# Kernel tuning notes

Hardware: AMD Instinct MI355X
Metric: run time of the kernel (lower is better)

Reference implementation:

```python
import jax, jax.numpy as jnp
import numpy as np

D_MODEL = 1024
N_HEADS = 16
HEAD_DIM = D_MODEL // N_HEADS
FF_DIM = 4096
EPS = 1e-5


def _layer_norm(v, g, b):
    mu = jnp.mean(v, axis=-1, keepdims=True)
    var = jnp.mean(jnp.square(v - mu), axis=-1, keepdims=True)
    return (v - mu) * jax.lax.rsqrt(var + EPS) * g + b


def setup_inputs() -> dict:
    key = jax.random.key(0)
    ks = jax.random.split(key, 16)
    s = 0.02
    x = jax.random.normal(ks[0], (2, 2048, D_MODEL), dtype=jnp.float32)
    Wq = jax.random.normal(ks[1], (D_MODEL, D_MODEL), dtype=jnp.float32) * s
    Wk = jax.random.normal(ks[2], (D_MODEL, D_MODEL), dtype=jnp.float32) * s
    Wv = jax.random.normal(ks[3], (D_MODEL, D_MODEL), dtype=jnp.float32) * s
    Wo = jax.random.normal(ks[4], (D_MODEL, D_MODEL), dtype=jnp.float32) * s
    bq = jnp.zeros((D_MODEL,), jnp.float32)
    bk = jnp.zeros((D_MODEL,), jnp.float32)
    bv = jnp.zeros((D_MODEL,), jnp.float32)
    bo = jnp.zeros((D_MODEL,), jnp.float32)
    # per-head Conv1d(kernel=1) == per-head linear; weights [H, out, in]
    W1 = jax.random.normal(ks[5], (N_HEADS, FF_DIM, HEAD_DIM), dtype=jnp.float32) * s
    b1 = jnp.zeros((N_HEADS, FF_DIM), jnp.float32)
    W2 = jax.random.normal(ks[6], (N_HEADS, HEAD_DIM, FF_DIM), dtype=jnp.float32) * s
    b2 = jnp.zeros((N_HEADS, HEAD_DIM), jnp.float32)
    g1 = jnp.ones((D_MODEL,), jnp.float32)
    be1 = jnp.zeros((D_MODEL,), jnp.float32)
    g2 = jnp.ones((D_MODEL,), jnp.float32)
    be2 = jnp.zeros((D_MODEL,), jnp.float32)
    return {"x": x, "Wq": Wq, "bq": bq, "Wk": Wk, "bk": bk, "Wv": Wv, "bv": bv,
            "Wo": Wo, "bo": bo, "W1": W1, "b1": b1, "W2": W2, "b2": b2,
            "g1": g1, "be1": be1, "g2": g2, "be2": be2}


def reference(x, Wq, bq, Wk, bk, Wv, bv, Wo, bo, W1, b1, W2, b2, g1, be1, g2, be2):
    B, S, D = x.shape
    H, hd = N_HEADS, HEAD_DIM
    # --- multi-head self-attention (standard scaled dot-product) ---
    q = (x @ Wq + bq).reshape(B, S, H, hd)
    k = (x @ Wk + bk).reshape(B, S, H, hd)
    v = (x @ Wv + bv).reshape(B, S, H, hd)
    scores = jnp.einsum('bqhd,bkhd->bhqk', q, k) / jnp.sqrt(jnp.float32(hd))
    attn = jax.nn.softmax(scores, axis=-1)          # [B,H,S,S]
    ctx = jnp.einsum('bhqk,bkhd->bqhd', attn, v).reshape(B, S, D)
    residual = ctx @ Wo + bo
    # dropout is identity in eval mode
    x1 = _layer_norm(x + residual, g1, be1)
    # --- per-head feed-forward (Conv1d kernel=1 per head, batched over heads) ---
    xh = x1.reshape(B, S, H, hd)
    h = jax.nn.relu(jnp.einsum('bshd,hfd->bshf', xh, W1) + b1)   # [B,S,H,FF]
    ff = jnp.einsum('bshf,hdf->bshd', h, W2) + b2                 # [B,S,H,hd]
    y = _layer_norm(x1 + ff.reshape(B, S, D), g2, be2)
    return (y, attn)
```

## Files before the change

### kernel.cpp

```cpp
#include <hip/hip_runtime.h>
#include <cstddef>

#define D_M 1024
#define NH 16
#define HD 64
#define FFD 4096
#define SQ 2048
#define BB 2
#define TOK (BB*SQ)
#define EPS 1e-5f

typedef __attribute__((ext_vector_type(8))) short bf16x8;
typedef __attribute__((ext_vector_type(4))) float f32x4;

__device__ inline unsigned short f32_bf16_rne(float f) {
  unsigned int u = __float_as_uint(f);
  unsigned int r = (u + 0x7fffu + ((u >> 16) & 1u)) >> 16;
  return (unsigned short)r;
}

__device__ inline float wave_sum(float v) {
  #pragma unroll
  for (int m = 32; m >= 1; m >>= 1) v += __shfl_xor(v, m);
  return v;
}

__global__ __launch_bounds__(256)
void convert2_bf16_k(const float* __restrict__ s0, unsigned short* __restrict__ d0,
                     const float* __restrict__ s1, unsigned short* __restrict__ d1, int n4) {
  const float* src = blockIdx.y ? s1 : s0;
  unsigned short* dst = blockIdx.y ? d1 : d0;
  int i = blockIdx.x * 256 + threadIdx.x;
  if (i >= n4) return;
  float4 v = ((const float4*)src)[i];
  ushort4 h;
  h.x = f32_bf16_rne(v.x); h.y = f32_bf16_rne(v.y);
  h.z = f32_bf16_rne(v.z); h.w = f32_bf16_rne(v.w);
  ((ushort4*)dst)[i] = h;
}

__global__ __launch_bounds__(256)
void convert_bf16_k(const float* __restrict__ src, unsigned short* __restrict__ dst, int n4) {
  int i = blockIdx.x * 256 + threadIdx.x;
  if (i >= n4) return;
  float4 v = ((const float4*)src)[i];
  ushort4 h;
  h.x = f32_bf16_rne(v.x); h.y = f32_bf16_rne(v.y);
  h.z = f32_bf16_rne(v.z); h.w = f32_bf16_rne(v.w);
  ((ushort4*)dst)[i] = h;
}

__global__ __launch_bounds__(256)
void transp4_k(const float* __restrict__ W0, const float* __restrict__ W1_,
               const float* __restrict__ W2_, const float* __restrict__ W3,
               unsigned short* __restrict__ h0, unsigned short* __restrict__ h1,
               unsigned short* __restrict__ h2, unsigned short* __restrict__ h3) {
  const float* W; unsigned short* hT;
  switch (blockIdx.z) {
    case 0: W = W0; hT = h0; break;
    case 1: W = W1_; hT = h1; break;
    case 2: W = W2_; hT = h2; break;
    default: W = W3; hT = h3; break;
  }
  __shared__ float tile[64][65];
  const int bn = blockIdx.x * 64;
  const int bk = blockIdx.y * 64;
  const int t = threadIdx.x;
  #pragma unroll
  for (int i = 0; i < 4; ++i) {
    int r = (t >> 4) + i * 16, c = (t & 15) * 4;
    float4 v = *(const float4*)&W[(size_t)(bk + r) * D_M + bn + c];
    tile[r][c] = v.x; tile[r][c + 1] = v.y; tile[r][c + 2] = v.z; tile[r][c + 3] = v.w;
  }
  __syncthreads();
  #pragma unroll
  for (int i = 0; i < 4; ++i) {
    int n = (t >> 4) + i * 16, k = (t & 15) * 4;
    ushort4 h;
    h.x = f32_bf16_rne(tile[k][n]);     h.y = f32_bf16_rne(tile[k + 1][n]);
    h.z = f32_bf16_rne(tile[k + 2][n]); h.w = f32_bf16_rne(tile[k + 3][n]);
    *(ushort4*)&hT[(size_t)(bn + n) * D_M + bk + k] = h;
  }
}

__global__ __launch_bounds__(256)
void qkv_gemm_k(const unsigned short* __restrict__ xh_g,
                const unsigned short* __restrict__ Bqh, const unsigned short* __restrict__ Bkh,
                const unsigned short* __restrict__ Bvh,
                const float* __restrict__ bq, const float* __restrict__ bk, const float* __restrict__ bv,
                unsigned short* __restrict__ qh, unsigned short* __restrict__ kh,
                unsigned short* __restrict__ vth) {
  constexpr int LDK = 40;
  __shared__ unsigned short Ah[64 * LDK];
  __shared__ unsigned short Bh[3][128 * LDK];
  const int tid = threadIdx.x;
  const int wave = tid >> 6, lane = tid & 63;
  const int wm = (wave >> 1) * 32, wn = (wave & 1) * 64;
  const int bn = blockIdx.x * 128, bm = blockIdx.y * 64;
  const int K = D_M;

  f32x4 acc[3][2][4] = {};
  const int sr = tid >> 2, sk = (tid & 3) * 8;
  const int l15 = lane & 15, k8 = (lane >> 4) * 8;

  const unsigned short* Bhp[3] = {Bqh, Bkh, Bvh};

  for (int k0 = 0; k0 < K; k0 += 32) {
    *(uint4*)&Ah[sr * LDK + sk] = *(const uint4*)&xh_g[(size_t)(bm + sr) * K + k0 + sk];
    #pragma unroll
    for (int s = 0; s < 3; ++s) {
      #pragma unroll
      for (int c = 0; c < 2; ++c) {
        int r = sr + c * 64;
        *(uint4*)&Bh[s][r * LDK + sk] = *(const uint4*)&Bhp[s][(size_t)(bn + r) * K + k0 + sk];
      }
    }
    __syncthreads();
    bf16x8 af[2];
    #pragma unroll
    for (int m = 0; m < 2; ++m)
      af[m] = *(bf16x8*)&Ah[(wm + m * 16 + l15) * LDK + k8];
    #pragma unroll
    for (int s = 0; s < 3; ++s) {
      #pragma unroll
      for (int n = 0; n < 4; ++n) {
        bf16x8 b0 = *(bf16x8*)&Bh[s][(wn + n * 16 + l15) * LDK + k8];
        #pragma unroll
        for (int m = 0; m < 2; ++m) {
          if (s == 2) {
            acc[s][m][n] = __builtin_amdgcn_mfma_f32_16x16x32_bf16(af[m], b0, acc[s][m][n], 0, 0, 0);
          } else {
            acc[s][m][n] = __builtin_amdgcn_mfma_f32_16x16x32_bf16(b0, af[m], acc[s][m][n], 0, 0, 0);
          }
        }
      }
    }
    __syncthreads();
  }
  const int kq4 = (lane >> 4) * 4;
  #pragma unroll
  for (int s = 0; s < 2; ++s) {
    const float* bias = (s == 0) ? bq : bk;
    unsigned short* oh = (s == 0) ? qh : kh;
    #pragma unroll
    for (int n = 0; n < 4; ++n) {
      int colb = bn + wn + n * 16 + kq4;
      float4 bv4 = *(const float4*)&bias[colb];
      #pragma unroll
      for (int m = 0; m < 2; ++m) {
        int tok = bm + wm + m * 16 + l15;
        ushort4 h;
        h.x = f32_bf16_rne(acc[s][m][n][0] + bv4.x);
        h.y = f32_bf16_rne(acc[s][m][n][1] + bv4.y);
        h.z = f32_bf16_rne(acc[s][m][n][2] + bv4.z);
        h.w = f32_bf16_rne(acc[s][m][n][3] + bv4.w);
        *(ushort4*)&oh[(size_t)tok * D_M + colb] = h;
      }
    }
  }
  #pragma unroll
  for (int n = 0; n < 4; ++n) {
    int col = bn + wn + n * 16 + l15;
    float bvv = bv[col];
    #pragma unroll
    for (int m = 0; m < 2; ++m) {
      int row0 = bm + wm + m * 16 + kq4;
      ushort4 hv;
      hv.x = f32_bf16_rne(acc[2][m][n][0] + bvv); hv.y = f32_bf16_rne(acc[2][m][n][1] + bvv);
      hv.z = f32_bf16_rne(acc[2][m][n][2] + bvv); hv.w = f32_bf16_rne(acc[2][m][n][3] + bvv);
      size_t idx = (((size_t)(row0 >> 11) * NH + (col >> 6)) * HD + (col & 63)) * SQ + (row0 & 2047);
      *(ushort4*)&vth[idx] = hv;
    }
  }
}

__global__ __launch_bounds__(256)
void proj_gemm_k(const unsigned short* __restrict__ Ah_g,
                 const unsigned short* __restrict__ Bh_g,
                 const float* __restrict__ bias, float* __restrict__ C,
                 int M, int N, int K) {
  constexpr int LDK = 40;
  __shared__ unsigned short Ah[64 * LDK];
  __shared__ unsigned short Bh[128 * LDK];
  const int tid = threadIdx.x;
  const int wave = tid >> 6, lane = tid & 63;
  const int wm = (wave >> 1) * 32, wn = (wave & 1) * 64;
  const int bn = blockIdx.x * 128, bm = blockIdx.y * 64;

  f32x4 acc[2][4] = {};
  const int sr = tid >> 2, sk = (tid & 3) * 8;
  const int l15 = lane & 15, k8 = (lane >> 4) * 8;

  for (int k0 = 0; k0 < K; k0 += 32) {
    *(uint4*)&Ah[sr * LDK + sk] = *(const uint4*)&Ah_g[(size_t)(bm + sr) * K + k0 + sk];
    #pragma unroll
    for (int c = 0; c < 2; ++c) {
      int r = sr + c * 64;
      *(uint4*)&Bh[r * LDK + sk] = *(const uint4*)&Bh_g[(size_t)(bn + r) * K + k0 + sk];
    }
    __syncthreads();
    bf16x8 af[2], bfr[4];
    #pragma unroll
    for (int m = 0; m < 2; ++m)
      af[m] = *(bf16x8*)&Ah[(wm + m * 16 + l15) * LDK + k8];
    #pragma unroll
    for (int n = 0; n < 4; ++n)
      bfr[n] = *(bf16x8*)&Bh[(wn + n * 16 + l15) * LDK + k8];
    #pragma unroll
    for (int m = 0; m < 2; ++m)
      #pragma unroll
      for (int n = 0; n < 4; ++n)
        acc[m][n] = __builtin_amdgcn_mfma_f32_16x16x32_bf16(bfr[n], af[m], acc[m][n], 0, 0, 0);
    __syncthreads();
  }
  const int kq4 = (lane >> 4) * 4;
  #pragma unroll
  for (int n = 0; n < 4; ++n) {
    int colb = bn + wn + n * 16 + kq4;
    float4 bv4 = *(const float4*)&bias[colb];
    #pragma unroll
    for (int m = 0; m < 2; ++m) {
      int tok = bm + wm + m * 16 + l15;
      float4 v = {acc[m][n][0] + bv4.x, acc[m][n][1] + bv4.y,
                  acc[m][n][2] + bv4.z, acc[m][n][3] + bv4.w};
      *(float4*)&C[(size_t)tok * N + colb] = v;
    }
  }
}

__global__ __launch_bounds__(256)
void fused_attn_k(const unsigned short* __restrict__ qh,
                  const unsigned short* __restrict__ kh,
                  const unsigned short* __restrict__ vth,
                  float* __restrict__ attn,
                  unsigned short* __restrict__ ctxh) {
  constexpr int LDK = 72;
  __shared__ unsigned short arena[6 * 64 * LDK];
  const int tid = threadIdx.x, wave = tid >> 6, lane = tid & 63;
  const int l15 = lane & 15, kq = lane >> 4;
  const int bh = blockIdx.x, b = bh >> 4, h = bh & 15;
  const int q0 = blockIdx.y * 128;

  bf16x8 qfh[2][2];
  #pragma unroll
  for (int qi = 0; qi < 2; ++qi) {
    const size_t qoff = (size_t)(b * SQ + q0 + wave * 32 + qi * 16 + l15) * D_M + h * HD + kq * 8;
    qfh[qi][0] = *(const bf16x8*)&qh[qoff];  qfh[qi][1] = *(const bf16x8*)&qh[qoff + 32];
  }

  const size_t kbase = (size_t)(b * SQ) * D_M + h * HD;
  const size_t vbase = (size_t)bh * HD * SQ;
  const int srow = tid >> 2, sc = (tid & 3) * 16;

  float lsum[2] = {0.f, 0.f};
  {
    #pragma unroll
    for (int hlf = 0; hlf < 2; ++hlf) {
      const int row = srow + hlf * 64;
      const unsigned short* src = &kh[kbase + (size_t)row * D_M + sc];
      *(uint4*)&arena[row * LDK + sc] = *(const uint4*)src;
      *(uint4*)&arena[row * LDK + sc + 8] = *(const uint4*)(src + 8);
    }
  }
  __syncthreads();
  for (int t = 0; t < SQ / 128; ++t) {
    const int abuf = (t & 1) * 9216;
    const bool pf = (t + 1 < SQ / 128);
    uint4 r0[2], r1[2];
    if (pf) {
      #pragma unroll
      for (int hlf = 0; hlf < 2; ++hlf) {
        const unsigned short* src = &kh[kbase + (size_t)((t + 1) * 128 + srow + hlf * 64) * D_M + sc];
        r0[hlf] = *(const uint4*)src;
        r1[hlf] = *(const uint4*)(src + 8);
      }
    }
    #pragma unroll
    for (int n = 0; n < 8; ++n) {
      bf16x8 kb0 = *(bf16x8*)&arena[abuf + (n * 16 + l15) * LDK + kq * 8];
      bf16x8 kb1 = *(bf16x8*)&arena[abuf + (n * 16 + l15) * LDK + 32 + kq * 8];
      #pragma unroll
      for (int qi = 0; qi < 2; ++qi) {
        f32x4 s = {};
        s = __builtin_amdgcn_mfma_f32_16x16x32_bf16(kb0, qfh[qi][0], s, 0, 0, 0);
        s = __builtin_amdgcn_mfma_f32_16x16x32_bf16(kb1, qfh[qi][1], s, 0, 0, 0);
        #pragma unroll
        for (int r = 0; r < 4; ++r) lsum[qi] += __expf(s[r] * 0.125f);
      }
    }
    if (pf) {
      const int nbuf = ((t + 1) & 1) * 9216;
      #pragma unroll
      for (int hlf = 0; hlf < 2; ++hlf) {
        const int row = srow + hlf * 64;
        *(uint4*)&arena[nbuf + row * LDK + sc] = r0[hlf];
        *(uint4*)&arena[nbuf + row * LDK + sc + 8] = r1[hlf];
      }
    }
    __syncthreads();
  }
  float invl[2];
  #pragma unroll
  for (int qi = 0; qi < 2; ++qi) {
    float l = lsum[qi];
    l += __shfl_xor(l, 16);
    l += __shfl_xor(l, 32);
    invl[qi] = 1.0f / l;
  }

  unsigned short* Ph = arena + 18432;
  f32x4 cacc[2][4] = {};
  {
    const unsigned short* srch = &kh[kbase + (size_t)srow * D_M + sc];
    const unsigned short* srcv = &vth[vbase + (size_t)srow * SQ + sc];
    *(uint4*)&arena[srow * LDK + sc] = *(const uint4*)srch;
    *(uint4*)&arena[srow * LDK + sc + 8] = *(const uint4*)(srch + 8);
    *(uint4*)&arena[9216 + srow * LDK + sc] = *(const uint4*)srcv;
    *(uint4*)&arena[9216 + srow * LDK + sc + 8] = *(const uint4*)(srcv + 8);
  }
  __syncthreads();
  for (int t = 0; t < SQ / 64; ++t) {
    const int kbuf = (t & 1) * 4608;
    const int vbuf = 9216 + (t & 1) * 4608;
    const int k0 = t * 64;
    const bool pf = (t + 1 < SQ / 64);
    uint4 rk0, rk1, rv0, rv1;
    if (pf) {
      const unsigned short* srch = &kh[kbase + (size_t)(k0 + 64 + srow) * D_M + sc];
      const unsigned short* srcv = &vth[vbase + (size_t)srow * SQ + k0 + 64 + sc];
      rk0 = *(const uint4*)srch; rk1 = *(const uint4*)(srch + 8);
      rv0 = *(const uint4*)srcv; rv1 = *(const uint4*)(srcv + 8);
    }
    #pragma unroll
    for (int n = 0; n < 4; ++n) {
      bf16x8 kb0 = *(bf16x8*)&arena[kbuf + (n * 16 + l15) * LDK + kq * 8];
      bf16x8 kb1 = *(bf16x8*)&arena[kbuf + (n * 16 + l15) * LDK + 32 + kq * 8];
      #pragma unroll
      for (int qi = 0; qi < 2; ++qi) {
        f32x4 s = {};
        s = __builtin_amdgcn_mfma_f32_16x16x32_bf16(kb0, qfh[qi][0], s, 0, 0, 0);
        s = __builtin_amdgcn_mfma_f32_16x16x32_bf16(kb1, qfh[qi][1], s, 0, 0, 0);
        float4 pv;
        pv.x = __expf(s[0] * 0.125f) * invl[qi];
        pv.y = __expf(s[1] * 0.125f) * invl[qi];
        pv.z = __expf(s[2] * 0.125f) * invl[qi];
        pv.w = __expf(s[3] * 0.125f) * invl[qi];
        const int qrow = wave * 32 + qi * 16 + l15;
        *(float4*)&attn[((size_t)bh * SQ + q0 + qrow) * SQ + k0 + n * 16 + kq * 4] = pv;
        ushort4 p4;
        p4.x = f32_bf16_rne(pv.x); p4.y = f32_bf16_rne(pv.y);
        p4.z = f32_bf16_rne(pv.z); p4.w = f32_bf16_rne(pv.w);
        *(ushort4*)&Ph[qrow * LDK + n * 16 + kq * 4] = p4;
      }
    }
    #pragma unroll
    for (int qi = 0; qi < 2; ++qi) {
      bf16x8 pa0 = *(bf16x8*)&Ph[(wave * 32 + qi * 16 + l15) * LDK + kq * 8];
      bf16x8 pa1 = *(bf16x8*)&Ph[(wave * 32 + qi * 16 + l15) * LDK + 32 + kq * 8];
      #pragma unroll
      for (int n = 0; n < 4; ++n) {
        bf16x8 vb0 = *(bf16x8*)&arena[vbuf + (n * 16 + l15) * LDK + kq * 8];
        bf16x8 vb1 = *(bf16x8*)&arena[vbuf + (n * 16 + l15) * LDK + 32 + kq * 8];
        cacc[qi][n] = __builtin_amdgcn_mfma_f32_16x16x32_bf16(vb0, pa0, cacc[qi][n], 0, 0, 0);
        cacc[qi][n] = __builtin_amdgcn_mfma_f32_16x16x32_bf16(vb1, pa1, cacc[qi][n], 0, 0, 0);
      }
    }
    if (pf) {
      const int nk = ((t + 1) & 1) * 4608;
      const int nv = 9216 + ((t + 1) & 1) * 4608;
      *(uint4*)&arena[nk + srow * LDK + sc] = rk0;
      *(uint4*)&arena[nk + srow * LDK + sc + 8] = rk1;
      *(uint4*)&arena[nv + srow * LDK + sc] = rv0;
      *(uint4*)&arena[nv + srow * LDK + sc + 8] = rv1;
    }
    __syncthreads();
  }
  #pragma unroll
  for (int qi = 0; qi < 2; ++qi)
    #pragma unroll
    for (int n = 0; n < 4; ++n) {
      ushort4 hh;
      hh.x = f32_bf16_rne(cacc[qi][n][0]); hh.y = f32_bf16_rne(cacc[qi][n][1]);
      hh.z = f32_bf16_rne(cacc[qi][n][2]); hh.w = f32_bf16_rne(cacc[qi][n][3]);
      size_t off = (size_t)(b * SQ + q0 + wave * 32 + qi * 16 + l15) * D_M + h * HD + n * 16 + kq * 4;
      *(ushort4*)&ctxh[off] = hh;
    }
}

__global__ __launch_bounds__(256)
void ff_bf16_k(const unsigned short* __restrict__ x1h,
               const unsigned short* __restrict__ W1h_, const float* __restrict__ b1,
               const unsigned short* __restrict__ W2h_, const float* __restrict__ b2,
               float* __restrict__ out) {
  constexpr int LDW = 72;
  constexpr int LDH = 40;
  __shared__ unsigned short W1sh[2][32 * LDW];
  __shared__ unsigned short W2sh[2][64 * LDH];
  __shared__ unsigned short Hh[128 * LDH];

  const int tid = threadIdx.x;
  const int wave = tid >> 6, lane = tid & 63;
  const int h = blockIdx.x;
  const int m0 = blockIdx.y * 128;
  const int l15 = lane & 15, kq = lane >> 4;

  const size_t w1base = (size_t)h * FFD * HD;
  const size_t w2base = (size_t)h * HD * FFD;
  const int r1 = tid >> 3, k1 = (tid & 7) * 8;
  const int r2 = tid >> 2, f2 = (tid & 3) * 8;

  bf16x8 xf[2][2];
  #pragma unroll
  for (int m = 0; m < 2; ++m)
    #pragma unroll
    for (int ks = 0; ks < 2; ++ks) {
      size_t gof = (size_t)(m0 + wave * 32 + m * 16 + l15) * D_M + h * HD + ks * 32 + kq * 8;
      xf[m][ks] = *(const bf16x8*)&x1h[gof];
    }

  {
    *(uint4*)&W1sh[0][r1 * LDW + k1] = *(const uint4*)&W1h_[w1base + (size_t)r1 * HD + k1];
    *(uint4*)&W2sh[0][r2 * LDH + f2] = *(const uint4*)&W2h_[w2base + (size_t)r2 * FFD + f2];
  }
  __syncthreads();

  f32x4 ffacc[2][4] = {};

  for (int ch = 0; ch < FFD / 32; ++ch) {
    const int buf = ch & 1;
    const bool pf = (ch + 1 < FFD / 32);
    uint4 w1h_r, w2h_r;
    if (pf) {
      const int f0n = (ch + 1) * 32;
      w1h_r = *(const uint4*)&W1h_[w1base + (size_t)(f0n + r1) * HD + k1];
      w2h_r = *(const uint4*)&W2h_[w2base + (size_t)r2 * FFD + f0n + f2];
    }
    f32x4 hacc[2][2] = {};
    #pragma unroll
    for (int ks = 0; ks < 2; ++ks) {
      #pragma unroll
      for (int nf = 0; nf < 2; ++nf) {
        bf16x8 w1f = *(bf16x8*)&W1sh[buf][(nf * 16 + l15) * LDW + ks * 32 + kq * 8];
        #pragma unroll
        for (int m = 0; m < 2; ++m)
          hacc[nf][m] = __builtin_amdgcn_mfma_f32_16x16x32_bf16(w1f, xf[m][ks], hacc[nf][m], 0, 0, 0);
      }
    }
    #pragma unroll
    for (int nf = 0; nf < 2; ++nf) {
      const int fb = nf * 16 + kq * 4;
      float4 b1v = *(const float4*)&b1[(size_t)h * FFD + ch * 32 + fb];
      #pragma unroll
      for (int m = 0; m < 2; ++m) {
        int tok = wave * 32 + m * 16 + l15;
        ushort4 hh;
        hh.x = f32_bf16_rne(fmaxf(hacc[nf][m][0] + b1v.x, 0.0f));
        hh.y = f32_bf16_rne(fmaxf(hacc[nf][m][1] + b1v.y, 0.0f));
        hh.z = f32_bf16_rne(fmaxf(hacc[nf][m][2] + b1v.z, 0.0f));
        hh.w = f32_bf16_rne(fmaxf(hacc[nf][m][3] + b1v.w, 0.0f));
        *(ushort4*)&Hh[tok * LDH + fb] = hh;
      }
    }
    bf16x8 hfr[2];
    #pragma unroll
    for (int m = 0; m < 2; ++m)
      hfr[m] = *(bf16x8*)&Hh[(wave * 32 + m * 16 + l15) * LDH + kq * 8];
    #pragma unroll
    for (int n = 0; n < 4; ++n) {
      bf16x8 w2f = *(bf16x8*)&W2sh[buf][(n * 16 + l15) * LDH + kq * 8];
      #pragma unroll
      for (int m = 0; m < 2; ++m)
        ffacc[m][n] = __builtin_amdgcn_mfma_f32_16x16x32_bf16(w2f, hfr[m], ffacc[m][n], 0, 0, 0);
    }
    if (pf) {
      *(uint4*)&W1sh[buf ^ 1][r1 * LDW + k1] = w1h_r;
      *(uint4*)&W2sh[buf ^ 1][r2 * LDH + f2] = w2h_r;
    }
    __syncthreads();
  }
  #pragma unroll
  for (int n = 0; n < 4; ++n) {
    int db = n * 16 + kq * 4;
    float4 b2v = *(const float4*)&b2[(size_t)h * HD + db];
    #pragma unroll
    for (int m = 0; m < 2; ++m) {
      int tok = m0 + wave * 32 + m * 16 + l15;
      float4 v = {ffacc[m][n][0] + b2v.x, ffacc[m][n][1] + b2v.y,
                  ffacc[m][n][2] + b2v.z, ffacc[m][n][3] + b2v.w};
      *(float4*)&out[(size_t)tok * D_M + h * HD + db] = v;
    }
  }
}

template<int BF16OUT>
__global__ __launch_bounds__(256)
void add_ln_kernel(const float* __restrict__ a, const float* __restrict__ r,
                   const float* __restrict__ g, const float* __restrict__ be,
                   float* __restrict__ out, unsigned short* __restrict__ oh) {
  const size_t row = blockIdx.x;
  const int tid = threadIdx.x;
  __shared__ float red1[4];
  __shared__ float red2[4];
  float4 va = ((const float4*)(a + row * D_M))[tid];
  float4 vr = ((const float4*)(r + row * D_M))[tid];
  float v0 = va.x + vr.x, v1 = va.y + vr.y, v2 = va.z + vr.z, v3 = va.w + vr.w;
  float s = v0 + v1 + v2 + v3;
  float sq = v0 * v0 + v1 * v1 + v2 * v2 + v3 * v3;
  s = wave_sum(s);
  sq = wave_sum(sq);
  if ((tid & 63) == 0) { red1[tid >> 6] = s; red2[tid >> 6] = sq; }
  __syncthreads();
  s = red1[0] + red1[1] + red1[2] + red1[3];
  sq = red2[0] + red2[1] + red2[2] + red2[3];
  const float mu = s * (1.0f / D_M);
  const float var = sq * (1.0f / D_M) - mu * mu;
  float x = var + EPS;
  float rs = rsqrtf(x);
  rs = rs * (1.5f - 0.5f * x * rs * rs);
  float4 gg = ((const float4*)g)[tid];
  float4 bb = ((const float4*)be)[tid];
  float4 o = {(v0 - mu) * rs * gg.x + bb.x, (v1 - mu) * rs * gg.y + bb.y,
              (v2 - mu) * rs * gg.z + bb.z, (v3 - mu) * rs * gg.w + bb.w};
  ((float4*)(out + row * D_M))[tid] = o;
  if (BF16OUT) {
    ushort4 h;
    h.x = f32_bf16_rne(o.x); h.y = f32_bf16_rne(o.y);
    h.z = f32_bf16_rne(o.z); h.w = f32_bf16_rne(o.w);
    ((ushort4*)(oh + row * D_M))[tid] = h;
  }
}

extern "C" void kernel_launch(void* const* d_in, const int* in_sizes, int n_in,
                              void* d_out, int out_size, void* d_ws, size_t ws_size,
                              hipStream_t stream) {
  const float* x   = (const float*)d_in[0];
  const float* Wq  = (const float*)d_in[1];
  const float* bq  = (const float*)d_in[2];
  const float* Wk  = (const float*)d_in[3];
  const float* bk  = (const float*)d_in[4];
  const float* Wv  = (const float*)d_in[5];
  const float* bv  = (const float*)d_in[6];
  const float* Wo  = (const float*)d_in[7];
  const float* bo  = (const float*)d_in[8];
  const float* W1  = (const float*)d_in[9];
  const float* b1  = (const float*)d_in[10];
  const float* W2  = (const float*)d_in[11];
  const float* b2  = (const float*)d_in[12];
  const float* g1  = (const float*)d_in[13];
  const float* be1 = (const float*)d_in[14];
  const float* g2  = (const float*)d_in[15];
  const float* be2 = (const float*)d_in[16];

  float* y_out = (float*)d_out;
  float* attn  = (float*)d_out + (size_t)TOK * D_M;

  char* p = (char*)d_ws;
  const size_t MB = 1024 * 1024;
  unsigned short* WqT = (unsigned short*)(p + 0 * MB);
  unsigned short* WkT = (unsigned short*)(p + 2 * MB);
  unsigned short* WvT = (unsigned short*)(p + 4 * MB);
  unsigned short* WoT = (unsigned short*)(p + 6 * MB);
  unsigned short* xh  = (unsigned short*)(p + 8 * MB);
  unsigned short* qh  = (unsigned short*)(p + 16 * MB);
  unsigned short* kh  = (unsigned short*)(p + 24 * MB);
  unsigned short* vth = (unsigned short*)(p + 32 * MB);
  unsigned short* ctxh = (unsigned short*)(p + 40 * MB);
  float* resid = (float*)(p + 48 * MB);
  float* x1b   = (float*)(p + 64 * MB);
  unsigned short* x1c_h = (unsigned short*)(p + 8 * MB);
  unsigned short* W1c_h = (unsigned short*)(p + 16 * MB);
  unsigned short* W2c_h = (unsigned short*)(p + 24 * MB);
  float* ffb = (float*)(p + 32 * MB);

  const dim3 blk(256);
  const int n4_act = TOK * D_M / 4;

  transp4_k<<<dim3(16, 16, 4), blk, 0, stream>>>(Wq, Wk, Wv, Wo, WqT, WkT, WvT, WoT);
  convert_bf16_k<<<dim3(n4_act / 256), blk, 0, stream>>>(x, xh, n4_act);

  qkv_gemm_k<<<dim3(D_M / 128, TOK / 64), blk, 0, stream>>>(
      xh, WqT, WkT, WvT, bq, bk, bv, qh, kh, vth);

  fused_attn_k<<<dim3(BB * NH, SQ / 128), blk, 0, stream>>>(qh, kh, vth, attn, ctxh);

  proj_gemm_k<<<dim3(D_M / 128, TOK / 64), blk, 0, stream>>>(
      ctxh, WoT, bo, resid, TOK, D_M, D_M);
  add_ln_kernel<1><<<dim3(TOK), blk, 0, stream>>>(x, resid, g1, be1, x1b, x1c_h);

  convert2_bf16_k<<<dim3(n4_act / 256, 2), blk, 0, stream>>>(W1, W1c_h, W2, W2c_h, n4_act);
  ff_bf16_k<<<dim3(NH, TOK / 128), blk, 0, stream>>>(x1c_h, W1c_h, b1, W2c_h, b2, ffb);
  add_ln_kernel<0><<<dim3(TOK), blk, 0, stream>>>(x1b, ffb, g2, be2, y_out, nullptr);
}
```

Baseline: 513.3 us.

## Repartition FF kernel waves into 2x2 grid over tokens and feature halves

```diff
diff --git a/kernel.cpp b/kernel.cpp
--- a/kernel.cpp
+++ b/kernel.cpp
@@ -26,10 +26,7 @@
 }
 
 __global__ __launch_bounds__(256)
-void convert2_bf16_k(const float* __restrict__ s0, unsigned short* __restrict__ d0,
-                     const float* __restrict__ s1, unsigned short* __restrict__ d1, int n4) {
-  const float* src = blockIdx.y ? s1 : s0;
-  unsigned short* dst = blockIdx.y ? d1 : d0;
+void convert_bf16_k(const float* __restrict__ src, unsigned short* __restrict__ dst, int n4) {
   int i = blockIdx.x * 256 + threadIdx.x;
   if (i >= n4) return;
   float4 v = ((const float4*)src)[i];
@@ -40,7 +37,10 @@
 }
 
 __global__ __launch_bounds__(256)
-void convert_bf16_k(const float* __restrict__ src, unsigned short* __restrict__ dst, int n4) {
+void convert2_bf16_k(const float* __restrict__ s0, unsigned short* __restrict__ d0,
+                     const float* __restrict__ s1, unsigned short* __restrict__ d1, int n4) {
+  const float* src = blockIdx.y ? s1 : s0;
+  unsigned short* dst = blockIdx.y ? d1 : d0;
   int i = blockIdx.x * 256 + threadIdx.x;
   if (i >= n4) return;
   float4 v = ((const float4*)src)[i];
@@ -400,6 +400,7 @@
 
   const int tid = threadIdx.x;
   const int wave = tid >> 6, lane = tid & 63;
+  const int wm = wave >> 1, wf = wave & 1, wd = wave & 1;
   const int h = blockIdx.x;
   const int m0 = blockIdx.y * 128;
   const int l15 = lane & 15, kq = lane >> 4;
@@ -409,12 +410,12 @@
   const int r1 = tid >> 3, k1 = (tid & 7) * 8;
   const int r2 = tid >> 2, f2 = (tid & 3) * 8;
 
-  bf16x8 xf[2][2];
-  #pragma unroll
-  for (int m = 0; m < 2; ++m)
+  bf16x8 xf[4][2];
+  #pragma unroll
+  for (int m = 0; m < 4; ++m)
     #pragma unroll
     for (int ks = 0; ks < 2; ++ks) {
-      size_t gof = (size_t)(m0 + wave * 32 + m * 16 + l15) * D_M + h * HD + ks * 32 + kq * 8;
+      size_t gof = (size_t)(m0 + wm * 64 + m * 16 + l15) * D_M + h * HD + ks * 32 + kq * 8;
       xf[m][ks] = *(const bf16x8*)&x1h[gof];
     }
 
@@ -424,7 +425,7 @@
   }
   __syncthreads();
 
-  f32x4 ffacc[2][4] = {};
+  f32x4 ffacc[4][2] = {};
 
   for (int ch = 0; ch < FFD / 32; ++ch) {
     const int buf = ch & 1;
@@ -435,42 +436,40 @@
       w1h_r = *(const uint4*)&W1h_[w1base + (size_t)(f0n + r1) * HD + k1];
       w2h_r = *(const uint4*)&W2h_[w2base + (size_t)r2 * FFD + f0n + f2];
     }
-    f32x4 hacc[2][2] = {};
+    f32x4 hacc[4] = {};
     #pragma unroll
     for (int ks = 0; ks < 2; ++ks) {
-      #pragma unroll
-      for (int nf = 0; nf < 2; ++nf) {
-        bf16x8 w1f = *(bf16x8*)&W1sh[buf][(nf * 16 + l15) * LDW + ks * 32 + kq * 8];
-        #pragma unroll
-        for (int m = 0; m < 2; ++m)
-          hacc[nf][m] = __builtin_amdgcn_mfma_f32_16x16x32_bf16(w1f, xf[m][ks], hacc[nf][m], 0, 0, 0);
-      }
-    }
-    #pragma unroll
-    for (int nf = 0; nf < 2; ++nf) {
-      const int fb = nf * 16 + kq * 4;
+      bf16x8 w1h = *(bf16x8*)&W1sh[buf][(wf * 16 + l15) * LDW + ks * 32 + kq * 8];
+      #pragma unroll
+      for (int m = 0; m < 4; ++m)
+        hacc[m] = __builtin_amdgcn_mfma_f32_16x16x32_bf16(w1h, xf[m][ks], hacc[m], 0, 0, 0);
+    }
+    {
+      const int fb = wf * 16 + kq * 4;
       float4 b1v = *(const float4*)&b1[(size_t)h * FFD + ch * 32 + fb];
-      #pragma unroll
-      for (int m = 0; m < 2; ++m) {
-        int tok = wave * 32 + m * 16 + l15;
+      const float bb[4] = {b1v.x, b1v.y, b1v.z, b1v.w};
+      #pragma unroll
+      for (int m = 0; m < 4; ++m) {
+        int tok = wm * 64 + m * 16 + l15;
         ushort4 hh;
-        hh.x = f32_bf16_rne(fmaxf(hacc[nf][m][0] + b1v.x, 0.0f));
-        hh.y = f32_bf16_rne(fmaxf(hacc[nf][m][1] + b1v.y, 0.0f));
-        hh.z = f32_bf16_rne(fmaxf(hacc[nf][m][2] + b1v.z, 0.0f));
-        hh.w = f32_bf16_rne(fmaxf(hacc[nf][m][3] + b1v.w, 0.0f));
+        hh.x = f32_bf16_rne(fmaxf(hacc[m][0] + bb[0], 0.0f));
+        hh.y = f32_bf16_rne(fmaxf(hacc[m][1] + bb[1], 0.0f));
+        hh.z = f32_bf16_rne(fmaxf(hacc[m][2] + bb[2], 0.0f));
+        hh.w = f32_bf16_rne(fmaxf(hacc[m][3] + bb[3], 0.0f));
         *(ushort4*)&Hh[tok * LDH + fb] = hh;
       }
     }
-    bf16x8 hfr[2];
-    #pragma unroll
-    for (int m = 0; m < 2; ++m)
-      hfr[m] = *(bf16x8*)&Hh[(wave * 32 + m * 16 + l15) * LDH + kq * 8];
-    #pragma unroll
-    for (int n = 0; n < 4; ++n) {
-      bf16x8 w2f = *(bf16x8*)&W2sh[buf][(n * 16 + l15) * LDH + kq * 8];
-      #pragma unroll
-      for (int m = 0; m < 2; ++m)
-        ffacc[m][n] = __builtin_amdgcn_mfma_f32_16x16x32_bf16(w2f, hfr[m], ffacc[m][n], 0, 0, 0);
+    __syncthreads();
+    bf16x8 hfr[4];
+    #pragma unroll
+    for (int m = 0; m < 4; ++m)
+      hfr[m] = *(bf16x8*)&Hh[(wm * 64 + m * 16 + l15) * LDH + kq * 8];
+    #pragma unroll
+    for (int n = 0; n < 2; ++n) {
+      bf16x8 w2h = *(bf16x8*)&W2sh[buf][(wd * 32 + n * 16 + l15) * LDH + kq * 8];
+      #pragma unroll
+      for (int m = 0; m < 4; ++m)
+        ffacc[m][n] = __builtin_amdgcn_mfma_f32_16x16x32_bf16(w2h, hfr[m], ffacc[m][n], 0, 0, 0);
     }
     if (pf) {
       *(uint4*)&W1sh[buf ^ 1][r1 * LDW + k1] = w1h_r;
@@ -479,12 +478,12 @@
     __syncthreads();
   }
   #pragma unroll
-  for (int n = 0; n < 4; ++n) {
-    int db = n * 16 + kq * 4;
+  for (int n = 0; n < 2; ++n) {
+    int db = wd * 32 + n * 16 + kq * 4;
     float4 b2v = *(const float4*)&b2[(size_t)h * HD + db];
     #pragma unroll
-    for (int m = 0; m < 2; ++m) {
-      int tok = m0 + wave * 32 + m * 16 + l15;
+    for (int m = 0; m < 4; ++m) {
+      int tok = m0 + wm * 64 + m * 16 + l15;
       float4 v = {ffacc[m][n][0] + b2v.x, ffacc[m][n][1] + b2v.y,
                   ffacc[m][n][2] + b2v.z, ffacc[m][n][3] + b2v.w};
       *(float4*)&out[(size_t)tok * D_M + h * HD + db] = v;
```

Result: faster. 478.1 us, median of 2 (-6.9%).
